# Optimization experiments

Measured on AMD Instinct MI355X. Metric: run time of the kernel, lower is better.

The kernel has to match this reference:

```python
import jax, jax.numpy as jnp
import numpy as np

E = 64        # num_experts
K = 6         # num_experts_per_tok
D = 2048      # hidden_size
F = 1408      # moe_intermediate_size (per expert)
NSH = 2       # num_shared_experts
FS = F * NSH  # shared-expert intermediate
T = 2048      # tokens (batch*seq flattened)
CAP = 512     # expert capacity; mean load T*K/E=192, CAP is >20 sigma above -> no drops


def setup_inputs() -> dict:
    key = jax.random.key(0)
    ks = jax.random.split(key, 9)
    s = 0.02
    return {
        "hidden_states": jax.random.normal(ks[0], (T, D), jnp.float32),
        "gate_w": jax.random.normal(ks[1], (E, D), jnp.float32) * s,
        "w_gate": jax.random.normal(ks[2], (E, D, F), jnp.float32) * s,
        "w_up": jax.random.normal(ks[3], (E, D, F), jnp.float32) * s,
        "w_down": jax.random.normal(ks[4], (E, F, D), jnp.float32) * s,
        "ws_gate": jax.random.normal(ks[5], (D, FS), jnp.float32) * s,
        "ws_up": jax.random.normal(ks[6], (D, FS), jnp.float32) * s,
        "ws_down": jax.random.normal(ks[7], (FS, D), jnp.float32) * s,
    }


def reference(hidden_states, gate_w, w_gate, w_up, w_down, ws_gate, ws_up, ws_down):
    x = hidden_states  # [T, D]
    n_tok = x.shape[0]

    # ---- gate: softmax -> top-k -> renormalize (bailing_moe norm_topk_prob) ----
    probs = jax.nn.softmax(x @ gate_w.T, axis=-1)           # [T, E]
    topw, topi = jax.lax.top_k(probs, K)                    # [T, K]
    topw = topw / jnp.sum(topw, axis=-1, keepdims=True)

    flat_e = topi.reshape(-1)                               # [T*K] expert id per assignment
    flat_w = topw.reshape(-1)                               # [T*K] combine weight
    tok = jnp.arange(n_tok * K) // K                        # [T*K] source token (idxs // k)

    # ---- dispatch: slot of each assignment within its expert (== sort-by-expert) ----
    onehot = jax.nn.one_hot(flat_e, E, dtype=jnp.int32)     # [T*K, E]
    slot = jnp.take_along_axis(jnp.cumsum(onehot, axis=0) - onehot,
                               flat_e[:, None], axis=1)[:, 0]  # [T*K]
    valid = slot < CAP                                      # all True given CAP margin
    slot_c = jnp.where(valid, slot, CAP - 1)

    xa = x[tok] * valid[:, None].astype(x.dtype)            # [T*K, D] gathered tokens
    buf = jnp.zeros((E, CAP, D), x.dtype).at[flat_e, slot_c].add(xa)  # [E, CAP, D]

    # ---- per-expert SwiGLU MLP as grouped GEMMs ----
    h = jax.nn.silu(jnp.einsum('ecd,edf->ecf', buf, w_gate)) \
        * jnp.einsum('ecd,edf->ecf', buf, w_up)             # [E, CAP, F]
    o = jnp.einsum('ecf,efd->ecd', h, w_down)               # [E, CAP, D]

    # ---- combine: weighted scatter-add back to tokens ----
    ya = o[flat_e, slot_c] * (flat_w * valid.astype(flat_w.dtype))[:, None]
    y = jax.ops.segment_sum(ya, tok, num_segments=n_tok)    # [T, D]

    # ---- shared experts (SwiGLU on identity) ----
    shared = (jax.nn.silu(x @ ws_gate) * (x @ ws_up)) @ ws_down
    return y + shared
```

## Files before the change

### kernel.cpp

```cpp
#include <hip/hip_runtime.h>
#include <hip/hip_bf16.h>
#include <cstdint>

typedef __attribute__((ext_vector_type(4))) float f4;
typedef __attribute__((ext_vector_type(4))) float f32x4;
typedef __attribute__((ext_vector_type(8))) __bf16 bf16x8;
typedef unsigned short ushort_t;
typedef unsigned int uint_t;

#define TTOK 2048
#define DDIM 2048
#define NEXP 64
#define TOPK 6
#define FDIM 1408
#define FSH  2816
#define NASSIGN (TTOK*TOPK)

#define SBAR()     __asm__ __volatile__("s_barrier" ::: "memory")
#define WAITVMC(N) __asm__ __volatile__("s_waitcnt vmcnt(" #N ")" ::: "memory")
#define WAITLG()   __asm__ __volatile__("s_waitcnt lgkmcnt(0)" ::: "memory")

__device__ __forceinline__ ushort_t f2bf(float f){
  uint_t u = __builtin_bit_cast(uint_t, f);
  u = (u + 0x7FFFu + ((u >> 16) & 1u)) >> 16;
  return (ushort_t)u;
}
__device__ __forceinline__ float bf2f(uint_t b){
  uint_t u = (b & 0xFFFFu) << 16;
  return __builtin_bit_cast(float, u);
}
__device__ __forceinline__ void gld_lds16(const void* g, void* l){
  __builtin_amdgcn_global_load_lds((const __attribute__((address_space(1))) uint_t*)g,
                                   (__attribute__((address_space(3))) uint_t*)l, 16, 0, 0);
}

__global__ __launch_bounds__(256) void gate_topk_kernel(
    const float* __restrict__ x, const float* __restrict__ gw,
    int* __restrict__ topi, float* __restrict__ topw)
{
  __shared__ float xs[4*2048];
  __shared__ float lg[4*64];
  int tid = threadIdx.x;
  int t0 = blockIdx.x*4;
  const f4* xg = (const f4*)(x + (size_t)t0*DDIM);
  f4* xsv = (f4*)xs;
  for (int i = tid; i < 2048; i += 256) xsv[i] = xg[i];
  __syncthreads();
  int g = tid >> 6, l = tid & 63;
  int c = l & 3, er = l >> 2;
  const f4* xrow = (const f4*)(xs + g*2048 + c*512);
  #pragma unroll
  for (int eo = 0; eo < 4; ++eo){
    int e = eo*16 + er;
    const f4* wrow = (const f4*)(gw + (size_t)e*DDIM + c*512);
    float d = 0.f;
    #pragma unroll 4
    for (int j = 0; j < 128; ++j){
      f4 w = wrow[j], a = xrow[j];
      d += w.x*a.x + w.y*a.y + w.z*a.z + w.w*a.w;
    }
    d += __shfl_xor(d, 1);
    d += __shfl_xor(d, 2);
    if (c == 0) lg[g*64 + e] = d;
  }
  __syncthreads();
  float mv = lg[g*64 + l];
  float sv[6]; int si[6];
  #pragma unroll
  for (int s = 0; s < 6; ++s){
    float bv = mv; int bi = l;
    for (int off = 32; off > 0; off >>= 1){
      float ov = __shfl_xor(bv, off);
      int oi = __shfl_xor(bi, off);
      if (ov > bv || (ov == bv && oi < bi)){ bv = ov; bi = oi; }
    }
    sv[s] = bv; si[s] = bi;
    if (l == bi) mv = -3.4e38f;
  }
  if (l == 0){
    float sum = 0.f, wv[6];
    #pragma unroll
    for (int s = 0; s < 6; ++s){ wv[s] = __expf(sv[s] - sv[0]); sum += wv[s]; }
    float inv = 1.f/sum;
    int t = t0 + g;
    #pragma unroll
    for (int s = 0; s < 6; ++s){ topi[t*6+s] = si[s]; topw[t*6+s] = wv[s]*inv; }
  }
}

__global__ __launch_bounds__(256) void xcast_kernel(const float* __restrict__ x, ushort_t* __restrict__ xb){
  size_t base = ((size_t)blockIdx.x*256 + threadIdx.x)*8;
  f4 a = *(const f4*)(x + base);
  f4 b = *(const f4*)(x + base + 4);
  uint4 r;
  r.x = f2bf(a.x) | ((uint_t)f2bf(a.y)<<16);
  r.y = f2bf(a.z) | ((uint_t)f2bf(a.w)<<16);
  r.z = f2bf(b.x) | ((uint_t)f2bf(b.y)<<16);
  r.w = f2bf(b.z) | ((uint_t)f2bf(b.w)<<16);
  *(uint4*)(xb + base) = r;
}

__global__ __launch_bounds__(256) void count_kernel(const int* __restrict__ topi, int* __restrict__ counts){
  int a = blockIdx.x*256 + threadIdx.x;
  if (a < NASSIGN) atomicAdd(&counts[topi[a]], 1);
}
__global__ void scan_kernel(const int* __restrict__ counts, int* __restrict__ offsets){
  if (threadIdx.x == 0){
    int s = 0;
    for (int e = 0; e < NEXP; ++e){ offsets[e] = s; s += counts[e]; }
    offsets[NEXP] = s;
  }
}
__global__ __launch_bounds__(256) void scatter_kernel(
    const int* __restrict__ topi, const float* __restrict__ topw,
    const int* __restrict__ offsets, int* __restrict__ cursor,
    int* __restrict__ row_token, float* __restrict__ row_w, int* __restrict__ row_assign)
{
  int a = blockIdx.x*256 + threadIdx.x;
  if (a < NASSIGN){
    int e = topi[a];
    int pos = atomicAdd(&cursor[e], 1);
    int r = offsets[e] + pos;
    row_token[r]  = a / 6;
    row_w[r]      = topw[a];
    row_assign[r] = a;
  }
}

__global__ __launch_bounds__(512, 4) void gemm_gateup_kernel(
    const ushort_t* __restrict__ A, const float* __restrict__ Bg0, const float* __restrict__ Bu0,
    ushort_t* __restrict__ H,
    const int* __restrict__ offsets, const int* __restrict__ row_token,
    const ushort_t* __restrict__ zerop,
    int N, int K, int lda, int n_mt, int n_nt, int Mfix)
{
  int nwg = gridDim.x;
  int chunk = nwg >> 3;
  int L = (blockIdx.x & 7)*chunk + (blockIdx.x >> 3);
  int e, mt, nt, row0, rowcnt;
  if (offsets){
    int per = n_mt*n_nt; e = L/per; int rem = L - e*per; mt = rem/n_nt; nt = rem - mt*n_nt;
    row0 = offsets[e]; rowcnt = offsets[e+1] - row0;
  } else { e = 0; nt = L/n_mt; mt = L - nt*n_mt; row0 = 0; rowcnt = Mfix; }
  int m0 = mt*256;
  if (m0 >= rowcnt) return;

  const float* Bg = Bg0 + (size_t)e*K*N + nt*32;
  const float* Bu = Bu0 + (size_t)e*K*N + nt*32;

  __shared__ ushort_t As[2][256*64];
  __shared__ ushort_t Bsh[2*2048];

  int tid = threadIdx.x;
  int lane = tid & 63;
  int w = tid >> 6;

  int aslot = (tid & 7) ^ ((tid >> 3) & 7) ^ ((tid >> 6) & 7);
  const ushort_t* asrc[4];
  #pragma unroll
  for (int i = 0; i < 4; ++i){
    int r = (tid >> 3) + i*64;
    int gr = m0 + r;
    bool v = gr < rowcnt;
    int tok = row_token ? (v ? row_token[row0+gr] : 0) : gr;
    const ushort_t* p = v ? (A + (size_t)tok*lda) : zerop;
    asrc[i] = p + aslot*8;
  }

  int half = tid >> 8;
  int l256 = tid & 255;
  int bn4 = l256 & 7, bk2 = l256 >> 3;
  const float* Bsrc = half ? Bu : Bg;
  int bdoff[4];
  #pragma unroll
  for (int j = 0; j < 4; ++j){
    int n = bn4*4 + j;
    int pchunk = ((bk2 >> 2) ^ (n & 7) ^ ((n >> 3) & 7)) & 7;
    bdoff[j] = half*2048 + n*64 + pchunk*8 + (bk2 & 3)*2;
  }

  f32x4 accG[2][2], accU[2][2];
  #pragma unroll
  for (int i=0;i<2;++i)
    #pragma unroll
    for (int j=0;j<2;++j){ accG[i][j] = f32x4{0.f,0.f,0.f,0.f}; accU[i][j] = f32x4{0.f,0.f,0.f,0.f}; }

  int nK = K >> 6;
  {
    const float* bp = Bsrc + (size_t)(bk2*2)*N + bn4*4;
    f4 v0 = *(const f4*)(bp);
    f4 v1 = *(const f4*)(bp + (size_t)N);
    #pragma unroll
    for (int i = 0; i < 4; ++i)
      gld_lds16(asrc[i], &As[0][i*4096 + tid*8]);
    #pragma unroll
    for (int j = 0; j < 4; ++j){
      uint_t pk = f2bf(v0[j]) | ((uint_t)f2bf(v1[j]) << 16);
      *(uint_t*)&Bsh[bdoff[j]] = pk;
    }
    WAITLG();
  }

  for (int ks = 0; ks < nK; ++ks){
    int cur = ks & 1, nxt = cur ^ 1;
    bool pf = (ks + 1) < nK;
    f4 v0, v1;
    if (pf){
      const float* bp = Bsrc + (size_t)(((ks + 1) << 6) + bk2*2)*N + bn4*4;
      v0 = *(const f4*)(bp);
      v1 = *(const f4*)(bp + (size_t)N);
      int k0n = (ks + 1) << 6;
      #pragma unroll
      for (int i = 0; i < 4; ++i)
        gld_lds16(asrc[i] + k0n, &As[nxt][i*4096 + tid*8]);
      WAITVMC(6);
    } else {
      WAITVMC(0);
    }
    SBAR();

    #pragma unroll
    for (int kk = 0; kk < 2; ++kk){
      bf16x8 af[2], bg[2], bu[2];
      int kb = (kk << 2) + (lane >> 4);
      #pragma unroll
      for (int i = 0; i < 2; ++i){
        int ar = w*32 + i*16 + (lane & 15);
        int ch = (kb ^ (ar & 7) ^ ((ar >> 3) & 7)) & 7;
        af[i] = *(const bf16x8*)&As[cur][ar*64 + (ch << 3)];
      }
      #pragma unroll
      for (int j = 0; j < 2; ++j){
        int br = j*16 + (lane & 15);
        int ch = (kb ^ (br & 7) ^ ((br >> 3) & 7)) & 7;
        bg[j] = *(const bf16x8*)&Bsh[br*64 + (ch << 3)];
        bu[j] = *(const bf16x8*)&Bsh[2048 + br*64 + (ch << 3)];
      }
      #pragma unroll
      for (int i = 0; i < 2; ++i)
        #pragma unroll
        for (int j = 0; j < 2; ++j){
          accG[i][j] = __builtin_amdgcn_mfma_f32_16x16x32_bf16(af[i], bg[j], accG[i][j], 0,0,0);
          accU[i][j] = __builtin_amdgcn_mfma_f32_16x16x32_bf16(af[i], bu[j], accU[i][j], 0,0,0);
        }
    }
    SBAR();
    if (pf){
      #pragma unroll
      for (int j = 0; j < 4; ++j){
        uint_t pk = f2bf(v0[j]) | ((uint_t)f2bf(v1[j]) << 16);
        *(uint_t*)&Bsh[bdoff[j]] = pk;
      }
      WAITLG();
    }
  }

  #pragma unroll
  for (int i = 0; i < 2; ++i)
    #pragma unroll
    for (int j = 0; j < 2; ++j){
      int col = nt*32 + j*16 + (lane & 15);
      #pragma unroll
      for (int q = 0; q < 4; ++q){
        int r = w*32 + i*16 + ((lane >> 4) << 2) + q;
        int gr = m0 + r;
        if (gr < rowcnt){
          float gv = accG[i][j][q];
          float uv = accU[i][j][q];
          float hv = (gv / (1.f + __expf(-gv))) * uv;
          H[(size_t)(row0 + gr)*(size_t)N + col] = f2bf(hv);
        }
      }
    }
}

__global__ __launch_bounds__(512, 4) void gemm_down_kernel(
    const ushort_t* __restrict__ A, const float* __restrict__ B0,
    ushort_t* __restrict__ outb, float* __restrict__ outf,
    const int* __restrict__ offsets, const float* __restrict__ row_w, const int* __restrict__ row_assign,
    const ushort_t* __restrict__ zerop,
    int N, int K, int lda, int n_mt, int n_nt, int Mfix)
{
  int nwg = gridDim.x;
  int chunk = nwg >> 3;
  int L = (blockIdx.x & 7)*chunk + (blockIdx.x >> 3);
  int e, mt, nt, row0, rowcnt;
  if (offsets){
    int per = n_mt*n_nt; e = L/per; int rem = L - e*per; mt = rem/n_nt; nt = rem - mt*n_nt;
    row0 = offsets[e]; rowcnt = offsets[e+1] - row0;
  } else { e = 0; nt = L/n_mt; mt = L - nt*n_mt; row0 = 0; rowcnt = Mfix; }
  int m0 = mt*256;
  if (m0 >= rowcnt) return;

  const float* B = B0 + (size_t)e*K*N + nt*64;

  __shared__ ushort_t As[2][256*64];
  __shared__ ushort_t Bs[64*64];
  __shared__ float Wr[256];
  __shared__ int Ar[256];

  int tid = threadIdx.x;
  int lane = tid & 63;
  int wid = tid >> 6;
  int wm = wid & 3, wn = wid >> 2;

  if (offsets){
    for (int t = tid; t < 256; t += 512){
      int gr = m0 + t;
      bool v = gr < rowcnt;
      Wr[t] = v ? row_w[row0+gr] : 0.f;
      Ar[t] = v ? row_assign[row0+gr] : 0;
    }
  }

  int aslot = (tid & 7) ^ ((tid >> 3) & 7) ^ ((tid >> 6) & 7);
  const ushort_t* asrc[4];
  #pragma unroll
  for (int i = 0; i < 4; ++i){
    int r = (tid >> 3) + i*64;
    int gr = m0 + r;
    bool v = gr < rowcnt;
    const ushort_t* p = v ? (A + (size_t)(row0+gr)*lda) : zerop;
    asrc[i] = p + aslot*8;
  }

  int bn4 = tid & 15, bk8 = tid >> 4;
  int bdoff[4];
  #pragma unroll
  for (int j = 0; j < 4; ++j){
    int n = bn4*4 + j;
    int pchunk = ((bk8 >> 2) ^ (n & 7) ^ ((n >> 3) & 7)) & 7;
    bdoff[j] = n*64 + pchunk*8 + (bk8 & 3)*2;
  }

  f32x4 acc[4][2];
  #pragma unroll
  for (int i=0;i<4;++i)
    #pragma unroll
    for (int j=0;j<2;++j) acc[i][j] = f32x4{0.f,0.f,0.f,0.f};

  int nK = K >> 6;
  {
    const float* bp = B + (size_t)(bk8*2)*N + bn4*4;
    f4 v0 = *(const f4*)(bp);
    f4 v1 = *(const f4*)(bp + (size_t)N);
    #pragma unroll
    for (int i = 0; i < 4; ++i)
      gld_lds16(asrc[i], &As[0][i*4096 + tid*8]);
    #pragma unroll
    for (int j = 0; j < 4; ++j){
      uint_t pk = f2bf(v0[j]) | ((uint_t)f2bf(v1[j]) << 16);
      *(uint_t*)&Bs[bdoff[j]] = pk;
    }
    WAITLG();
  }

  for (int ks = 0; ks < nK; ++ks){
    int cur = ks & 1, nxt = cur ^ 1;
    bool pf = (ks + 1) < nK;
    f4 v0, v1;
    if (pf){
      const float* bp = B + (size_t)(((ks + 1) << 6) + bk8*2)*N + bn4*4;
      v0 = *(const f4*)(bp);
      v1 = *(const f4*)(bp + (size_t)N);
      int k0n = (ks + 1) << 6;
      #pragma unroll
      for (int i = 0; i < 4; ++i)
        gld_lds16(asrc[i] + k0n, &As[nxt][i*4096 + tid*8]);
      WAITVMC(6);
    } else {
      WAITVMC(0);
    }
    SBAR();

    #pragma unroll
    for (int kk = 0; kk < 2; ++kk){
      bf16x8 af[4], bb[2];
      int kb = (kk << 2) + (lane >> 4);
      #pragma unroll
      for (int i = 0; i < 4; ++i){
        int ar = wm*64 + i*16 + (lane & 15);
        int ch = (kb ^ (ar & 7) ^ ((ar >> 3) & 7)) & 7;
        af[i] = *(const bf16x8*)&As[cur][ar*64 + (ch << 3)];
      }
      #pragma unroll
      for (int j = 0; j < 2; ++j){
        int br = wn*32 + j*16 + (lane & 15);
        int ch = (kb ^ (br & 7) ^ ((br >> 3) & 7)) & 7;
        bb[j] = *(const bf16x8*)&Bs[br*64 + (ch << 3)];
      }
      #pragma unroll
      for (int i = 0; i < 4; ++i)
        #pragma unroll
        for (int j = 0; j < 2; ++j)
          acc[i][j] = __builtin_amdgcn_mfma_f32_16x16x32_bf16(af[i], bb[j], acc[i][j], 0,0,0);
    }
    SBAR();
    if (pf){
      #pragma unroll
      for (int j = 0; j < 4; ++j){
        uint_t pk = f2bf(v0[j]) | ((uint_t)f2bf(v1[j]) << 16);
        *(uint_t*)&Bs[bdoff[j]] = pk;
      }
      WAITLG();
    }
  }

  #pragma unroll
  for (int i = 0; i < 4; ++i)
    #pragma unroll
    for (int j = 0; j < 2; ++j){
      int col = nt*64 + wn*32 + j*16 + (lane & 15);
      #pragma unroll
      for (int q = 0; q < 4; ++q){
        int r = wm*64 + i*16 + ((lane >> 4) << 2) + q;
        int gr = m0 + r;
        if (gr < rowcnt){
          float val = acc[i][j][q];
          if (offsets){
            outb[(size_t)Ar[r]*2048 + col] = f2bf(val * Wr[r]);
          } else {
            outf[(size_t)gr*2048 + col] = val;
          }
        }
      }
    }
}

__global__ __launch_bounds__(256) void combine_kernel(const ushort_t* __restrict__ oa, float* __restrict__ out){
  size_t base = ((size_t)blockIdx.x*256 + threadIdx.x)*8;
  int t = (int)(base >> 11);
  int d = (int)(base & 2047);
  f4 s0 = *(const f4*)(out + base);
  f4 s1 = *(const f4*)(out + base + 4);
  #pragma unroll
  for (int k = 0; k < 6; ++k){
    const ushort_t* row = oa + (((size_t)(t*6+k)) << 11) + d;
    uint4 u = *(const uint4*)row;
    s0.x += bf2f(u.x); s0.y += bf2f(u.x >> 16);
    s0.z += bf2f(u.y); s0.w += bf2f(u.y >> 16);
    s1.x += bf2f(u.z); s1.y += bf2f(u.z >> 16);
    s1.z += bf2f(u.w); s1.w += bf2f(u.w >> 16);
  }
  *(f4*)(out + base) = s0;
  *(f4*)(out + base + 4) = s1;
}

extern "C" void kernel_launch(void* const* d_in, const int* in_sizes, int n_in,
                              void* d_out, int out_size, void* d_ws, size_t ws_size,
                              hipStream_t stream)
{
  const float* x       = (const float*)d_in[0];
  const float* gate_w  = (const float*)d_in[1];
  const float* w_gate  = (const float*)d_in[2];
  const float* w_up    = (const float*)d_in[3];
  const float* w_down  = (const float*)d_in[4];
  const float* ws_gate = (const float*)d_in[5];
  const float* ws_up   = (const float*)d_in[6];
  const float* ws_down = (const float*)d_in[7];
  float* out = (float*)d_out;

  char* ws = (char*)d_ws;
  int*      topi       = (int*)(ws + 0);
  float*    topw       = (float*)(ws + 49152);
  int*      counts     = (int*)(ws + 98304);
  int*      cursor     = (int*)(ws + 98560);
  int*      offsets    = (int*)(ws + 98816);
  int*      row_token  = (int*)(ws + 99328);
  float*    row_w      = (float*)(ws + 148480);
  int*      row_assign = (int*)(ws + 197632);
  ushort_t* zerop      = (ushort_t*)(ws + 262144);
  ushort_t* xb         = (ushort_t*)(ws + 524288);
  ushort_t* Hbuf       = (ushort_t*)(ws + 8912896);
  ushort_t* Shbuf      = (ushort_t*)(ws + 43515904);
  ushort_t* oa         = (ushort_t*)(ws + 55050240);
  (void)ws_size; (void)in_sizes; (void)n_in; (void)out_size;

  hipMemsetAsync(ws + 98304, 0, 512, stream);
  hipMemsetAsync(zerop, 0, 8192, stream);

  gate_topk_kernel<<<512, 256, 0, stream>>>(x, gate_w, topi, topw);
  xcast_kernel<<<2048, 256, 0, stream>>>(x, xb);
  count_kernel<<<48, 256, 0, stream>>>(topi, counts);
  scan_kernel<<<1, 64, 0, stream>>>(counts, offsets);
  scatter_kernel<<<48, 256, 0, stream>>>(topi, topw, offsets, cursor, row_token, row_w, row_assign);

  gemm_gateup_kernel<<<5632, 512, 0, stream>>>(xb, w_gate, w_up, Hbuf, offsets, row_token, zerop,
                                               FDIM, DDIM, DDIM, 2, 44, 0);
  gemm_gateup_kernel<<<704, 512, 0, stream>>>(xb, ws_gate, ws_up, Shbuf, nullptr, nullptr, zerop,
                                              FSH, DDIM, DDIM, 8, 88, TTOK);
  gemm_down_kernel<<<256, 512, 0, stream>>>(Shbuf, ws_down, nullptr, out, nullptr, nullptr, nullptr, zerop,
                                            DDIM, FSH, FSH, 8, 32, TTOK);
  gemm_down_kernel<<<4096, 512, 0, stream>>>(Hbuf, w_down, oa, nullptr, offsets, row_w, row_assign, zerop,
                                             DDIM, FDIM, FDIM, 2, 32, 0);
  combine_kernel<<<2048, 256, 0, stream>>>(oa, out);
}
```

Before: 986.2 us.

## Split fused gate/up GEMM into separate passes with larger 256x128 tiles

The fused gate+up GEMM, which used 256x32 tiles per projection, is replaced by a generic x@W kernel. It runs twice: first the gate projection is written to a bf16 buffer, then the up pass reads that buffer back and applies SiLU(g)*u in its epilogue. Both this kernel and the down GEMM move to 1024-thread blocks with 256x128 tiles. The goal is to raise A-tile reuse across N and cut redundant token-gather traffic. The cost is an extra bf16 write and read of the gate intermediate, twice as many GEMM launches for gate/up, and fewer workgroups per launch.

```diff
diff --git a/kernel.cpp b/kernel.cpp
--- a/kernel.cpp
+++ b/kernel.cpp
@@ -127,15 +127,14 @@
   }
 }
 
-__global__ __launch_bounds__(512, 4) void gemm_gateup_kernel(
-    const ushort_t* __restrict__ A, const float* __restrict__ Bg0, const float* __restrict__ Bu0,
-    ushort_t* __restrict__ H,
+__global__ __launch_bounds__(1024, 4) void gemm_xw_kernel(
+    const ushort_t* __restrict__ A, const float* __restrict__ B0,
+    const ushort_t* __restrict__ gsrc, ushort_t* __restrict__ H,
     const int* __restrict__ offsets, const int* __restrict__ row_token,
     const ushort_t* __restrict__ zerop,
     int N, int K, int lda, int n_mt, int n_nt, int Mfix)
 {
-  int nwg = gridDim.x;
-  int chunk = nwg >> 3;
+  int nwg = gridDim.x, chunk = nwg >> 3;
   int L = (blockIdx.x & 7)*chunk + (blockIdx.x >> 3);
   int e, mt, nt, row0, rowcnt;
   if (offsets){
@@ -145,21 +144,21 @@
   int m0 = mt*256;
   if (m0 >= rowcnt) return;
 
-  const float* Bg = Bg0 + (size_t)e*K*N + nt*32;
-  const float* Bu = Bu0 + (size_t)e*K*N + nt*32;
+  const float* B = B0 + (size_t)e*K*N + nt*128;
 
   __shared__ ushort_t As[2][256*64];
-  __shared__ ushort_t Bsh[2*2048];
+  __shared__ ushort_t Bsh[128*64];
 
   int tid = threadIdx.x;
   int lane = tid & 63;
-  int w = tid >> 6;
+  int wid = tid >> 6;
+  int wm = wid >> 2, wn = wid & 3;
 
   int aslot = (tid & 7) ^ ((tid >> 3) & 7) ^ ((tid >> 6) & 7);
-  const ushort_t* asrc[4];
-  #pragma unroll
-  for (int i = 0; i < 4; ++i){
-    int r = (tid >> 3) + i*64;
+  const ushort_t* asrc[2];
+  #pragma unroll
+  for (int i = 0; i < 2; ++i){
+    int r = (tid >> 3) + i*128;
     int gr = m0 + r;
     bool v = gr < rowcnt;
     int tok = row_token ? (v ? row_token[row0+gr] : 0) : gr;
@@ -167,32 +166,29 @@
     asrc[i] = p + aslot*8;
   }
 
-  int half = tid >> 8;
-  int l256 = tid & 255;
-  int bn4 = l256 & 7, bk2 = l256 >> 3;
-  const float* Bsrc = half ? Bu : Bg;
+  int bn4 = tid & 31, bk2 = tid >> 5;
+  const float* bbase = B + (size_t)(bk2*2)*N + bn4*4;
   int bdoff[4];
   #pragma unroll
   for (int j = 0; j < 4; ++j){
     int n = bn4*4 + j;
-    int pchunk = ((bk2 >> 2) ^ (n & 7) ^ ((n >> 3) & 7)) & 7;
-    bdoff[j] = half*2048 + n*64 + pchunk*8 + (bk2 & 3)*2;
-  }
-
-  f32x4 accG[2][2], accU[2][2];
-  #pragma unroll
-  for (int i=0;i<2;++i)
-    #pragma unroll
-    for (int j=0;j<2;++j){ accG[i][j] = f32x4{0.f,0.f,0.f,0.f}; accU[i][j] = f32x4{0.f,0.f,0.f,0.f}; }
+    int ch = ((bk2 >> 2) ^ (n & 7) ^ ((n >> 3) & 7)) & 7;
+    bdoff[j] = n*64 + ch*8 + (bk2 & 3)*2;
+  }
+
+  f32x4 acc[4][2];
+  #pragma unroll
+  for (int i=0;i<4;++i)
+    #pragma unroll
+    for (int j=0;j<2;++j) acc[i][j] = f32x4{0.f,0.f,0.f,0.f};
 
   int nK = K >> 6;
   {
-    const float* bp = Bsrc + (size_t)(bk2*2)*N + bn4*4;
-    f4 v0 = *(const f4*)(bp);
-    f4 v1 = *(const f4*)(bp + (size_t)N);
-    #pragma unroll
-    for (int i = 0; i < 4; ++i)
-      gld_lds16(asrc[i], &As[0][i*4096 + tid*8]);
+    f4 v0 = *(const f4*)(bbase);
+    f4 v1 = *(const f4*)(bbase + (size_t)N);
+    #pragma unroll
+    for (int i = 0; i < 2; ++i)
+      gld_lds16(asrc[i], &As[0][i*8192 + tid*8]);
     #pragma unroll
     for (int j = 0; j < 4; ++j){
       uint_t pk = f2bf(v0[j]) | ((uint_t)f2bf(v1[j]) << 16);
@@ -206,14 +202,14 @@
     bool pf = (ks + 1) < nK;
     f4 v0, v1;
     if (pf){
-      const float* bp = Bsrc + (size_t)(((ks + 1) << 6) + bk2*2)*N + bn4*4;
+      const float* bp = bbase + (size_t)((ks + 1) << 6)*N;
       v0 = *(const f4*)(bp);
       v1 = *(const f4*)(bp + (size_t)N);
       int k0n = (ks + 1) << 6;
       #pragma unroll
-      for (int i = 0; i < 4; ++i)
-        gld_lds16(asrc[i] + k0n, &As[nxt][i*4096 + tid*8]);
-      WAITVMC(6);
+      for (int i = 0; i < 2; ++i)
+        gld_lds16(asrc[i] + k0n, &As[nxt][i*8192 + tid*8]);
+      WAITVMC(4);
     } else {
       WAITVMC(0);
     }
@@ -221,28 +217,25 @@
 
     #pragma unroll
     for (int kk = 0; kk < 2; ++kk){
-      bf16x8 af[2], bg[2], bu[2];
+      bf16x8 af[4], bb[2];
       int kb = (kk << 2) + (lane >> 4);
       #pragma unroll
-      for (int i = 0; i < 2; ++i){
-        int ar = w*32 + i*16 + (lane & 15);
+      for (int i = 0; i < 4; ++i){
+        int ar = wm*64 + i*16 + (lane & 15);
         int ch = (kb ^ (ar & 7) ^ ((ar >> 3) & 7)) & 7;
         af[i] = *(const bf16x8*)&As[cur][ar*64 + (ch << 3)];
       }
       #pragma unroll
       for (int j = 0; j < 2; ++j){
-        int br = j*16 + (lane & 15);
+        int br = wn*32 + j*16 + (lane & 15);
         int ch = (kb ^ (br & 7) ^ ((br >> 3) & 7)) & 7;
-        bg[j] = *(const bf16x8*)&Bsh[br*64 + (ch << 3)];
-        bu[j] = *(const bf16x8*)&Bsh[2048 + br*64 + (ch << 3)];
-      }
-      #pragma unroll
-      for (int i = 0; i < 2; ++i)
+        bb[j] = *(const bf16x8*)&Bsh[br*64 + (ch << 3)];
+      }
+      #pragma unroll
+      for (int i = 0; i < 4; ++i)
         #pragma unroll
-        for (int j = 0; j < 2; ++j){
-          accG[i][j] = __builtin_amdgcn_mfma_f32_16x16x32_bf16(af[i], bg[j], accG[i][j], 0,0,0);
-          accU[i][j] = __builtin_amdgcn_mfma_f32_16x16x32_bf16(af[i], bu[j], accU[i][j], 0,0,0);
-        }
+        for (int j = 0; j < 2; ++j)
+          acc[i][j] = __builtin_amdgcn_mfma_f32_16x16x32_bf16(af[i], bb[j], acc[i][j], 0,0,0);
     }
     SBAR();
     if (pf){
@@ -256,33 +249,35 @@
   }
 
   #pragma unroll
-  for (int i = 0; i < 2; ++i)
+  for (int i = 0; i < 4; ++i)
     #pragma unroll
     for (int j = 0; j < 2; ++j){
-      int col = nt*32 + j*16 + (lane & 15);
+      int col = nt*128 + wn*32 + j*16 + (lane & 15);
       #pragma unroll
       for (int q = 0; q < 4; ++q){
-        int r = w*32 + i*16 + ((lane >> 4) << 2) + q;
+        int r = wm*64 + i*16 + ((lane >> 4) << 2) + q;
         int gr = m0 + r;
         if (gr < rowcnt){
-          float gv = accG[i][j][q];
-          float uv = accU[i][j][q];
-          float hv = (gv / (1.f + __expf(-gv))) * uv;
-          H[(size_t)(row0 + gr)*(size_t)N + col] = f2bf(hv);
+          float val = acc[i][j][q];
+          size_t idx = (size_t)(row0 + gr)*(size_t)N + col;
+          if (gsrc){
+            float g = bf2f(gsrc[idx]);
+            val = (g / (1.f + __expf(-g))) * val;
+          }
+          H[idx] = f2bf(val);
         }
       }
     }
 }
 
-__global__ __launch_bounds__(512, 4) void gemm_down_kernel(
+__global__ __launch_bounds__(1024, 4) void gemm_down_kernel(
     const ushort_t* __restrict__ A, const float* __restrict__ B0,
     ushort_t* __restrict__ outb, float* __restrict__ outf,
     const int* __restrict__ offsets, const float* __restrict__ row_w, const int* __restrict__ row_assign,
     const ushort_t* __restrict__ zerop,
     int N, int K, int lda, int n_mt, int n_nt, int Mfix)
 {
-  int nwg = gridDim.x;
-  int chunk = nwg >> 3;
+  int nwg = gridDim.x, chunk = nwg >> 3;
   int L = (blockIdx.x & 7)*chunk + (blockIdx.x >> 3);
   int e, mt, nt, row0, rowcnt;
   if (offsets){
@@ -292,45 +287,44 @@
   int m0 = mt*256;
   if (m0 >= rowcnt) return;
 
-  const float* B = B0 + (size_t)e*K*N + nt*64;
+  const float* B = B0 + (size_t)e*K*N + nt*128;
 
   __shared__ ushort_t As[2][256*64];
-  __shared__ ushort_t Bs[64*64];
+  __shared__ ushort_t Bsh[128*64];
   __shared__ float Wr[256];
   __shared__ int Ar[256];
 
   int tid = threadIdx.x;
   int lane = tid & 63;
   int wid = tid >> 6;
-  int wm = wid & 3, wn = wid >> 2;
-
-  if (offsets){
-    for (int t = tid; t < 256; t += 512){
-      int gr = m0 + t;
-      bool v = gr < rowcnt;
-      Wr[t] = v ? row_w[row0+gr] : 0.f;
-      Ar[t] = v ? row_assign[row0+gr] : 0;
-    }
+  int wm = wid >> 2, wn = wid & 3;
+
+  if (offsets && tid < 256){
+    int gr = m0 + tid;
+    bool v = gr < rowcnt;
+    Wr[tid] = v ? row_w[row0+gr] : 0.f;
+    Ar[tid] = v ? row_assign[row0+gr] : 0;
   }
 
   int aslot = (tid & 7) ^ ((tid >> 3) & 7) ^ ((tid >> 6) & 7);
-  const ushort_t* asrc[4];
-  #pragma unroll
-  for (int i = 0; i < 4; ++i){
-    int r = (tid >> 3) + i*64;
+  const ushort_t* asrc[2];
+  #pragma unroll
+  for (int i = 0; i < 2; ++i){
+    int r = (tid >> 3) + i*128;
     int gr = m0 + r;
     bool v = gr < rowcnt;
     const ushort_t* p = v ? (A + (size_t)(row0+gr)*lda) : zerop;
     asrc[i] = p + aslot*8;
   }
 
-  int bn4 = tid & 15, bk8 = tid >> 4;
+  int bn4 = tid & 31, bk2 = tid >> 5;
+  const float* bbase = B + (size_t)(bk2*2)*N + bn4*4;
   int bdoff[4];
   #pragma unroll
   for (int j = 0; j < 4; ++j){
     int n = bn4*4 + j;
-    int pchunk = ((bk8 >> 2) ^ (n & 7) ^ ((n >> 3) & 7)) & 7;
-    bdoff[j] = n*64 + pchunk*8 + (bk8 & 3)*2;
+    int ch = ((bk2 >> 2) ^ (n & 7) ^ ((n >> 3) & 7)) & 7;
+    bdoff[j] = n*64 + ch*8 + (bk2 & 3)*2;
   }
 
   f32x4 acc[4][2];
@@ -341,16 +335,15 @@
 
   int nK = K >> 6;
   {
-    const float* bp = B + (size_t)(bk8*2)*N + bn4*4;
-    f4 v0 = *(const f4*)(bp);
-    f4 v1 = *(const f4*)(bp + (size_t)N);
-    #pragma unroll
-    for (int i = 0; i < 4; ++i)
-      gld_lds16(asrc[i], &As[0][i*4096 + tid*8]);
+    f4 v0 = *(const f4*)(bbase);
+    f4 v1 = *(const f4*)(bbase + (size_t)N);
+    #pragma unroll
+    for (int i = 0; i < 2; ++i)
+      gld_lds16(asrc[i], &As[0][i*8192 + tid*8]);
     #pragma unroll
     for (int j = 0; j < 4; ++j){
       uint_t pk = f2bf(v0[j]) | ((uint_t)f2bf(v1[j]) << 16);
-      *(uint_t*)&Bs[bdoff[j]] = pk;
+      *(uint_t*)&Bsh[bdoff[j]] = pk;
     }
     WAITLG();
   }
@@ -360,14 +353,14 @@
     bool pf = (ks + 1) < nK;
     f4 v0, v1;
     if (pf){
-      const float* bp = B + (size_t)(((ks + 1) << 6) + bk8*2)*N + bn4*4;
+      const float* bp = bbase + (size_t)((ks + 1) << 6)*N;
       v0 = *(const f4*)(bp);
       v1 = *(const f4*)(bp + (size_t)N);
       int k0n = (ks + 1) << 6;
       #pragma unroll
-      for (int i = 0; i < 4; ++i)
-        gld_lds16(asrc[i] + k0n, &As[nxt][i*4096 + tid*8]);
-      WAITVMC(6);
+      for (int i = 0; i < 2; ++i)
+        gld_lds16(asrc[i] + k0n, &As[nxt][i*8192 + tid*8]);
+      WAITVMC(4);
     } else {
       WAITVMC(0);
     }
@@ -387,7 +380,7 @@
       for (int j = 0; j < 2; ++j){
         int br = wn*32 + j*16 + (lane & 15);
         int ch = (kb ^ (br & 7) ^ ((br >> 3) & 7)) & 7;
-        bb[j] = *(const bf16x8*)&Bs[br*64 + (ch << 3)];
+        bb[j] = *(const bf16x8*)&Bsh[br*64 + (ch << 3)];
       }
       #pragma unroll
       for (int i = 0; i < 4; ++i)
@@ -400,7 +393,7 @@
       #pragma unroll
       for (int j = 0; j < 4; ++j){
         uint_t pk = f2bf(v0[j]) | ((uint_t)f2bf(v1[j]) << 16);
-        *(uint_t*)&Bs[bdoff[j]] = pk;
+        *(uint_t*)&Bsh[bdoff[j]] = pk;
       }
       WAITLG();
     }
@@ -410,7 +403,7 @@
   for (int i = 0; i < 4; ++i)
     #pragma unroll
     for (int j = 0; j < 2; ++j){
-      int col = nt*64 + wn*32 + j*16 + (lane & 15);
+      int col = nt*128 + wn*32 + j*16 + (lane & 15);
       #pragma unroll
       for (int q = 0; q < 4; ++q){
         int r = wm*64 + i*16 + ((lane >> 4) << 2) + q;
@@ -474,6 +467,8 @@
   ushort_t* Hbuf       = (ushort_t*)(ws + 8912896);
   ushort_t* Shbuf      = (ushort_t*)(ws + 43515904);
   ushort_t* oa         = (ushort_t*)(ws + 55050240);
+  ushort_t* Gbuf = oa;
+  ushort_t* GS   = (ushort_t*)(ws + 55050240 + 34603008);
   (void)ws_size; (void)in_sizes; (void)n_in; (void)out_size;
 
   hipMemsetAsync(ws + 98304, 0, 512, stream);
@@ -485,13 +480,17 @@
   scan_kernel<<<1, 64, 0, stream>>>(counts, offsets);
   scatter_kernel<<<48, 256, 0, stream>>>(topi, topw, offsets, cursor, row_token, row_w, row_assign);
 
-  gemm_gateup_kernel<<<5632, 512, 0, stream>>>(xb, w_gate, w_up, Hbuf, offsets, row_token, zerop,
-                                               FDIM, DDIM, DDIM, 2, 44, 0);
-  gemm_gateup_kernel<<<704, 512, 0, stream>>>(xb, ws_gate, ws_up, Shbuf, nullptr, nullptr, zerop,
-                                              FSH, DDIM, DDIM, 8, 88, TTOK);
-  gemm_down_kernel<<<256, 512, 0, stream>>>(Shbuf, ws_down, nullptr, out, nullptr, nullptr, nullptr, zerop,
-                                            DDIM, FSH, FSH, 8, 32, TTOK);
-  gemm_down_kernel<<<4096, 512, 0, stream>>>(Hbuf, w_down, oa, nullptr, offsets, row_w, row_assign, zerop,
-                                             DDIM, FDIM, FDIM, 2, 32, 0);
+  gemm_xw_kernel<<<1408, 1024, 0, stream>>>(xb, w_gate, nullptr, Gbuf, offsets, row_token, zerop,
+                                            FDIM, DDIM, DDIM, 2, 11, 0);
+  gemm_xw_kernel<<<176, 1024, 0, stream>>>(xb, ws_gate, nullptr, GS, nullptr, nullptr, zerop,
+                                           FSH, DDIM, DDIM, 8, 22, TTOK);
+  gemm_xw_kernel<<<1408, 1024, 0, stream>>>(xb, w_up, Gbuf, Hbuf, offsets, row_token, zerop,
+                                            FDIM, DDIM, DDIM, 2, 11, 0);
+  gemm_xw_kernel<<<176, 1024, 0, stream>>>(xb, ws_up, GS, Shbuf, nullptr, nullptr, zerop,
+                                           FSH, DDIM, DDIM, 8, 22, TTOK);
+  gemm_down_kernel<<<128, 1024, 0, stream>>>(Shbuf, ws_down, nullptr, out, nullptr, nullptr, nullptr, zerop,
+                                             DDIM, FSH, FSH, 8, 16, TTOK);
+  gemm_down_kernel<<<2048, 1024, 0, stream>>>(Hbuf, w_down, oa, nullptr, offsets, row_w, row_assign, zerop,
+                                              DDIM, FDIM, FDIM, 2, 16, 0);
   combine_kernel<<<2048, 256, 0, stream>>>(oa, out);
 }
```

After: 1.064 ms. 7.9% more time.
